# Kernel optimization log

Hardware: AMD Instinct MI355X
Metric: run time of the kernel (lower is better)

Reference implementation:

```python
import jax, jax.numpy as jnp
import numpy as np

N = 50000      # atoms
E = 800000     # edges (avg degree 32)
H = 64         # hidden_channels
F = 64         # num_filters
G = 50         # num_gaussians
L = 6          # num_interactions
B = 128        # graphs in batch
MAX_Z = 100
CUTOFF = 10.0


def setup_inputs() -> dict:
    key = jax.random.key(0)
    ks = jax.random.split(key, 20)
    s = 0.05  # weight scale
    return {
        "z": jax.random.randint(ks[0], (N,), 0, MAX_Z, dtype=jnp.int32),
        "pos": jax.random.uniform(ks[1], (N, 3), dtype=jnp.float32) * 5.0,
        "batch": jnp.sort(jax.random.randint(ks[2], (N,), 0, B, dtype=jnp.int32)),
        "edge_index": jax.random.randint(ks[3], (2, E), 0, N, dtype=jnp.int32),
        "embed": jax.random.normal(ks[4], (MAX_Z, H), dtype=jnp.float32) * s,
        "mlp_w1": jax.random.normal(ks[5], (L, G, F), dtype=jnp.float32) * s,
        "mlp_b1": jax.random.normal(ks[6], (L, F), dtype=jnp.float32) * s,
        "mlp_w2": jax.random.normal(ks[7], (L, F, F), dtype=jnp.float32) * s,
        "mlp_b2": jax.random.normal(ks[8], (L, F), dtype=jnp.float32) * s,
        "lin_w": jax.random.normal(ks[9], (L, H, F), dtype=jnp.float32) * s,
        "lin_out_w": jax.random.normal(ks[10], (L, F, H), dtype=jnp.float32) * s,
        "lin_out_b": jax.random.normal(ks[11], (L, H), dtype=jnp.float32) * s,
        "fc1_w": jax.random.normal(ks[12], (H, H // 2), dtype=jnp.float32) * s,
        "fc1_b": jax.random.normal(ks[13], (H // 2,), dtype=jnp.float32) * s,
        "fc2_w": jax.random.normal(ks[14], (H // 2, 1), dtype=jnp.float32) * s,
        "fc2_b": jax.random.normal(ks[15], (1,), dtype=jnp.float32) * s,
    }


def reference(z, pos, batch, edge_index, embed, mlp_w1, mlp_b1, mlp_w2, mlp_b2,
              lin_w, lin_out_w, lin_out_b, fc1_w, fc1_b, fc2_w, fc2_b):
    src, dst = edge_index[0], edge_index[1]
    # edge distances (replaces the python cdist loop; edge list is precomputed)
    d = jnp.sqrt(jnp.sum((pos[src] - pos[dst]) ** 2, axis=-1))  # [E]
    # Gaussian smearing
    offset = jnp.linspace(0.0, CUTOFF, G)
    coeff = -0.5 / (offset[1] - offset[0]) ** 2
    edge_attr = jnp.exp(coeff * (d[:, None] - offset) ** 2)  # [E, G]
    # cosine cutoff
    cut = 0.5 * (jnp.cos(d * np.pi / CUTOFF) + 1.0) * (d < CUTOFF).astype(d.dtype)  # [E]

    h = embed[z]  # [N, H]
    for l in range(L):
        # filter MLP on edge features, modulated by cutoff
        W = jnp.tanh(edge_attr @ mlp_w1[l] + mlp_b1[l]) @ mlp_w2[l] + mlp_b2[l]  # [E, F]
        W = W * cut[:, None]
        h_j = h @ lin_w[l]  # [N, F]
        messages = h_j[src] * W  # gather + modulate  [E, F]
        agg = jax.ops.segment_sum(messages, dst, num_segments=N)  # scatter-add [N, F]
        h = h + (agg @ lin_out_w[l] + lin_out_b[l])  # residual

    # global mean pool over graphs
    sums = jax.ops.segment_sum(h, batch, num_segments=B)  # [B, H]
    cnt = jax.ops.segment_sum(jnp.ones((h.shape[0],), h.dtype), batch, num_segments=B)
    pooled = sums / jnp.maximum(cnt, 1.0)[:, None]

    x = jax.nn.relu(pooled @ fc1_w + fc1_b)  # dropout = identity (eval)
    return x @ fc2_w + fc2_b  # [B, 1]
```

## Files before the change

kernel.cpp:

```cpp
#include <hip/hip_runtime.h>
#include <math.h>

#define E_EDGES 800000
#define N_ATOMS 50000
#define N_GRAPH 128
#define P_TBL   4096
#define SCAN_NB 49

static constexpr float PI_F   = 3.14159265358979323846f;
static constexpr float GSTEP  = 10.0f / 49.0f;
static constexpr float GCOEFF = -0.5f / (GSTEP * GSTEP);
static constexpr float DMAX   = 8.6603f;
static constexpr float DSCALE = (float)(P_TBL - 1) / DMAX;

__global__ void hist_kernel(const int* __restrict__ dst, int* __restrict__ cnt) {
    int e = blockIdx.x * 256 + threadIdx.x;
    if (e < E_EDGES) atomicAdd(&cnt[dst[e]], 1);
}

__global__ __launch_bounds__(1024)
void scan1_kernel(const int* __restrict__ cnt, int* __restrict__ local_ex,
                  int* __restrict__ bsum) {
    __shared__ int sh[1024];
    const int t = threadIdx.x;
    const int i = blockIdx.x * 1024 + t;
    const int v = (i < N_ATOMS) ? cnt[i] : 0;
    sh[t] = v;
    __syncthreads();
    #pragma unroll
    for (int off = 1; off < 1024; off <<= 1) {
        int u = (t >= off) ? sh[t - off] : 0;
        __syncthreads();
        sh[t] += u;
        __syncthreads();
    }
    if (i < N_ATOMS) local_ex[i] = sh[t] - v;
    if (t == 1023) bsum[blockIdx.x] = sh[t];
}

__global__ __launch_bounds__(1024)
void scan2_kernel(const int* __restrict__ local_ex, const int* __restrict__ bsum,
                  int* __restrict__ starts, int* __restrict__ cursor) {
    __shared__ int off;
    const int b = blockIdx.x;
    if (threadIdx.x < 64) {
        int v = (threadIdx.x < b) ? bsum[threadIdx.x] : 0;
        #pragma unroll
        for (int d = 32; d > 0; d >>= 1) v += __shfl_down(v, d, 64);
        if (threadIdx.x == 0) off = v;
    }
    __syncthreads();
    const int i = b * 1024 + threadIdx.x;
    if (i < N_ATOMS) {
        int v = local_ex[i] + off;
        starts[i] = v;
        cursor[i] = v;
    }
}

__global__ void scatter_kernel(const int* __restrict__ ei, const float* __restrict__ pos,
                               int* __restrict__ cursor, uint2* __restrict__ pk) {
    int e = blockIdx.x * 256 + threadIdx.x;
    if (e >= E_EDGES) return;
    int sidx = ei[e];
    int dd   = ei[E_EDGES + e];
    float dx = pos[3*sidx+0] - pos[3*dd+0];
    float dy = pos[3*sidx+1] - pos[3*dd+1];
    float dz = pos[3*sidx+2] - pos[3*dd+2];
    float dist = sqrtf(dx*dx + dy*dy + dz*dz);
    int p = atomicAdd(&cursor[dd], 1);
    pk[p] = make_uint2((unsigned)sidx, __float_as_uint(dist));
}

__global__ __launch_bounds__(256)
void table_kernel(const float* __restrict__ w1, const float* __restrict__ b1,
                  const float* __restrict__ w2, const float* __restrict__ b2,
                  float* __restrict__ tbl) {
    __shared__ float sa[4][52];
    __shared__ float st[4][64];
    const int l  = blockIdx.x >> 10;
    const int rb = blockIdx.x & 1023;
    const int rr = threadIdx.x >> 6;
    const int f  = threadIdx.x & 63;
    const int r  = rb * 4 + rr;
    const float dp = (float)r * (DMAX / (float)(P_TBL - 1));

    if (f < 50) {
        float t = dp - (float)f * GSTEP;
        sa[rr][f] = expf(GCOEFF * t * t);
    }
    __syncthreads();

    const float* W1 = w1 + (size_t)l * 50 * 64;
    const float* W2 = w2 + (size_t)l * 64 * 64;
    float t = b1[l * 64 + f];
    #pragma unroll 5
    for (int g = 0; g < 50; ++g) t = fmaf(sa[rr][g], W1[g * 64 + f], t);
    st[rr][f] = tanhf(t);
    __syncthreads();

    float w = b2[l * 64 + f];
    #pragma unroll 8
    for (int k = 0; k < 64; ++k) w = fmaf(st[rr][k], W2[k * 64 + f], w);
    float cutv = 0.5f * (cosf(dp * (PI_F / 10.0f)) + 1.0f);
    tbl[((size_t)l * P_TBL + r) * 64 + f] = w * cutv;
}

__global__ __launch_bounds__(256)
void embed_lin0_kernel(const int* __restrict__ z, const float* __restrict__ embed,
                       const float* __restrict__ W,
                       float* __restrict__ h, float* __restrict__ hj) {
    __shared__ float sA[64 * 65];
    __shared__ float sW[64 * 64];
    const int tid = threadIdx.x;
    const int rbase = blockIdx.x * 64;

    for (int i = tid; i < 64 * 64; i += 256) sW[i] = W[i];
    for (int i = tid; i < 64 * 64; i += 256) {
        int r = i >> 6, k = i & 63;
        int row = rbase + r;
        float v = 0.0f;
        if (row < N_ATOMS) {
            v = embed[(size_t)z[row] * 64 + k];
            h[(size_t)row * 64 + k] = v;
        }
        sA[r * 65 + k] = v;
    }
    __syncthreads();

    const int f0 = (tid & 7) * 8;
    const int r0 = (tid >> 3) * 2;
    float acc[2][8];
    #pragma unroll
    for (int i = 0; i < 2; ++i)
        #pragma unroll
        for (int j = 0; j < 8; ++j) acc[i][j] = 0.0f;

    #pragma unroll 4
    for (int k = 0; k < 64; ++k) {
        float a[2] = { sA[(r0+0)*65 + k], sA[(r0+1)*65 + k] };
        float4 wa = *(const float4*)&sW[k * 64 + f0];
        float4 wb = *(const float4*)&sW[k * 64 + f0 + 4];
        float w[8] = {wa.x, wa.y, wa.z, wa.w, wb.x, wb.y, wb.z, wb.w};
        #pragma unroll
        for (int i = 0; i < 2; ++i)
            #pragma unroll
            for (int j = 0; j < 8; ++j)
                acc[i][j] = fmaf(a[i], w[j], acc[i][j]);
    }

    #pragma unroll
    for (int i = 0; i < 2; ++i) {
        int row = rbase + r0 + i;
        if (row < N_ATOMS) {
            float* o = hj + (size_t)row * 64;
            *(float4*)&o[f0]     = make_float4(acc[i][0], acc[i][1], acc[i][2], acc[i][3]);
            *(float4*)&o[f0 + 4] = make_float4(acc[i][4], acc[i][5], acc[i][6], acc[i][7]);
        }
    }
}

__device__ __forceinline__ float edge_w(const float* __restrict__ tbl, float dist, int f) {
    float x = dist * DSCALE;
    int i0 = (int)x; i0 = (i0 > P_TBL - 2) ? (P_TBL - 2) : i0;
    float fr = x - (float)i0;
    float t0 = tbl[i0 * 64 + f];
    float t1 = tbl[i0 * 64 + 64 + f];
    return fmaf(fr, t1 - t0, t0);
}

__global__ __launch_bounds__(256)
void agg_kernel(const uint2* __restrict__ pk,
                const int* __restrict__ starts, const int* __restrict__ cnts,
                const float* __restrict__ hj, const float* __restrict__ tbl,
                float* __restrict__ agg) {
    const int f = threadIdx.x & 63;
    const int n = blockIdx.x * 4 + (threadIdx.x >> 6);
    if (n >= N_ATOMS) return;
    const int s   = starts[n];
    const int end = s + cnts[n];
    float a0 = 0.0f, a1 = 0.0f, a2 = 0.0f, a3 = 0.0f;
    float a4 = 0.0f, a5 = 0.0f, a6 = 0.0f, a7 = 0.0f;
    int e = s;
    for (; e + 8 <= end; e += 8) {
        uint2 p0 = pk[e+0], p1 = pk[e+1], p2 = pk[e+2], p3 = pk[e+3];
        uint2 p4 = pk[e+4], p5 = pk[e+5], p6 = pk[e+6], p7 = pk[e+7];
        float w0 = edge_w(tbl, __uint_as_float(p0.y), f);
        float w1 = edge_w(tbl, __uint_as_float(p1.y), f);
        float w2 = edge_w(tbl, __uint_as_float(p2.y), f);
        float w3 = edge_w(tbl, __uint_as_float(p3.y), f);
        float w4 = edge_w(tbl, __uint_as_float(p4.y), f);
        float w5 = edge_w(tbl, __uint_as_float(p5.y), f);
        float w6 = edge_w(tbl, __uint_as_float(p6.y), f);
        float w7 = edge_w(tbl, __uint_as_float(p7.y), f);
        a0 = fmaf(w0, hj[(size_t)p0.x * 64 + f], a0);
        a1 = fmaf(w1, hj[(size_t)p1.x * 64 + f], a1);
        a2 = fmaf(w2, hj[(size_t)p2.x * 64 + f], a2);
        a3 = fmaf(w3, hj[(size_t)p3.x * 64 + f], a3);
        a4 = fmaf(w4, hj[(size_t)p4.x * 64 + f], a4);
        a5 = fmaf(w5, hj[(size_t)p5.x * 64 + f], a5);
        a6 = fmaf(w6, hj[(size_t)p6.x * 64 + f], a6);
        a7 = fmaf(w7, hj[(size_t)p7.x * 64 + f], a7);
    }
    for (; e + 2 <= end; e += 2) {
        uint2 p0 = pk[e], p1 = pk[e+1];
        float w0 = edge_w(tbl, __uint_as_float(p0.y), f);
        float w1 = edge_w(tbl, __uint_as_float(p1.y), f);
        a0 = fmaf(w0, hj[(size_t)p0.x * 64 + f], a0);
        a1 = fmaf(w1, hj[(size_t)p1.x * 64 + f], a1);
    }
    if (e < end) {
        uint2 p0 = pk[e];
        float w0 = edge_w(tbl, __uint_as_float(p0.y), f);
        a0 = fmaf(w0, hj[(size_t)p0.x * 64 + f], a0);
    }
    agg[(size_t)n * 64 + f] = ((a0 + a1) + (a2 + a3)) + ((a4 + a5) + (a6 + a7));
}

__global__ __launch_bounds__(256)
void update_kernel(const float* __restrict__ agg,
                   const float* __restrict__ Wout, const float* __restrict__ bout,
                   float* __restrict__ h,
                   const float* __restrict__ Wlin, float* __restrict__ hj,
                   int doLin) {
    __shared__ float sA[64 * 65];
    __shared__ float sW[64 * 64];
    __shared__ float sb[64];
    const int tid = threadIdx.x;
    const int rbase = blockIdx.x * 64;

    for (int i = tid; i < 64 * 64; i += 256) sW[i] = Wout[i];
    if (tid < 64) sb[tid] = bout[tid];
    for (int i = tid; i < 64 * 64; i += 256) {
        int r = i >> 6, k = i & 63;
        int row = rbase + r;
        sA[r * 65 + k] = (row < N_ATOMS) ? agg[(size_t)row * 64 + k] : 0.0f;
    }
    __syncthreads();

    const int f0 = (tid & 7) * 8;
    const int r0 = (tid >> 3) * 2;

    float acc[2][8];
    #pragma unroll
    for (int i = 0; i < 2; ++i) {
        int row = rbase + r0 + i;
        if (row < N_ATOMS) {
            const float* hr = h + (size_t)row * 64;
            float4 h0 = *(const float4*)&hr[f0];
            float4 h1 = *(const float4*)&hr[f0 + 4];
            acc[i][0] = h0.x + sb[f0+0]; acc[i][1] = h0.y + sb[f0+1];
            acc[i][2] = h0.z + sb[f0+2]; acc[i][3] = h0.w + sb[f0+3];
            acc[i][4] = h1.x + sb[f0+4]; acc[i][5] = h1.y + sb[f0+5];
            acc[i][6] = h1.z + sb[f0+6]; acc[i][7] = h1.w + sb[f0+7];
        } else {
            #pragma unroll
            for (int j = 0; j < 8; ++j) acc[i][j] = 0.0f;
        }
    }

    #pragma unroll 4
    for (int k = 0; k < 64; ++k) {
        float a[2] = { sA[(r0+0)*65 + k], sA[(r0+1)*65 + k] };
        float4 wa = *(const float4*)&sW[k * 64 + f0];
        float4 wb = *(const float4*)&sW[k * 64 + f0 + 4];
        float w[8] = {wa.x, wa.y, wa.z, wa.w, wb.x, wb.y, wb.z, wb.w};
        #pragma unroll
        for (int i = 0; i < 2; ++i)
            #pragma unroll
            for (int j = 0; j < 8; ++j)
                acc[i][j] = fmaf(a[i], w[j], acc[i][j]);
    }
    __syncthreads();

    #pragma unroll
    for (int i = 0; i < 2; ++i) {
        int row = rbase + r0 + i;
        if (row < N_ATOMS) {
            float* o = h + (size_t)row * 64;
            *(float4*)&o[f0]     = make_float4(acc[i][0], acc[i][1], acc[i][2], acc[i][3]);
            *(float4*)&o[f0 + 4] = make_float4(acc[i][4], acc[i][5], acc[i][6], acc[i][7]);
        }
        #pragma unroll
        for (int j = 0; j < 8; ++j)
            sA[(r0 + i) * 65 + f0 + j] = acc[i][j];
    }
    if (!doLin) return;
    for (int i = tid; i < 64 * 64; i += 256) sW[i] = Wlin[i];
    __syncthreads();

    float acc2[2][8];
    #pragma unroll
    for (int i = 0; i < 2; ++i)
        #pragma unroll
        for (int j = 0; j < 8; ++j) acc2[i][j] = 0.0f;

    #pragma unroll 4
    for (int k = 0; k < 64; ++k) {
        float a[2] = { sA[(r0+0)*65 + k], sA[(r0+1)*65 + k] };
        float4 wa = *(const float4*)&sW[k * 64 + f0];
        float4 wb = *(const float4*)&sW[k * 64 + f0 + 4];
        float w[8] = {wa.x, wa.y, wa.z, wa.w, wb.x, wb.y, wb.z, wb.w};
        #pragma unroll
        for (int i = 0; i < 2; ++i)
            #pragma unroll
            for (int j = 0; j < 8; ++j)
                acc2[i][j] = fmaf(a[i], w[j], acc2[i][j]);
    }

    #pragma unroll
    for (int i = 0; i < 2; ++i) {
        int row = rbase + r0 + i;
        if (row < N_ATOMS) {
            float* o = hj + (size_t)row * 64;
            *(float4*)&o[f0]     = make_float4(acc2[i][0], acc2[i][1], acc2[i][2], acc2[i][3]);
            *(float4*)&o[f0 + 4] = make_float4(acc2[i][4], acc2[i][5], acc2[i][6], acc2[i][7]);
        }
    }
}

__global__ __launch_bounds__(256)
void pool_head_kernel(const float* __restrict__ h, const int* __restrict__ batch,
                      const float* __restrict__ fc1w, const float* __restrict__ fc1b,
                      const float* __restrict__ fc2w, const float* __restrict__ fc2b,
                      float* __restrict__ out) {
    __shared__ float part[4][64];
    __shared__ float sp[64];
    __shared__ float sx[32];
    __shared__ int bounds[2];
    const int g   = blockIdx.x;
    const int tid = threadIdx.x;

    if (tid < 2) {
        int target = g + tid;
        int lo = 0, hi = N_ATOMS;
        while (lo < hi) {
            int m = (lo + hi) >> 1;
            if (batch[m] < target) lo = m + 1; else hi = m;
        }
        bounds[tid] = lo;
    }
    __syncthreads();
    const int s = bounds[0], epos = bounds[1];

    const int f = tid & 63, wv = tid >> 6;
    float a = 0.0f;
    for (int r = s + wv; r < epos; r += 4) a += h[(size_t)r * 64 + f];
    part[wv][f] = a;
    __syncthreads();

    if (tid < 64) {
        float cnt = (float)(epos - s);
        sp[tid] = (part[0][tid] + part[1][tid] + part[2][tid] + part[3][tid])
                  / fmaxf(cnt, 1.0f);
    }
    __syncthreads();
    if (tid < 32) {
        float a1 = fc1b[tid];
        #pragma unroll 8
        for (int k = 0; k < 64; ++k) a1 = fmaf(sp[k], fc1w[k * 32 + tid], a1);
        sx[tid] = fmaxf(a1, 0.0f);
    }
    __syncthreads();
    if (tid == 0) {
        float a2 = fc2b[0];
        #pragma unroll 8
        for (int j = 0; j < 32; ++j) a2 = fmaf(sx[j], fc2w[j], a2);
        out[g] = a2;
    }
}

extern "C" void kernel_launch(void* const* d_in, const int* in_sizes, int n_in,
                              void* d_out, int out_size, void* d_ws, size_t ws_size,
                              hipStream_t stream) {
    const int*   z         = (const int*)  d_in[0];
    const float* pos       = (const float*)d_in[1];
    const int*   batch     = (const int*)  d_in[2];
    const int*   ei        = (const int*)  d_in[3];
    const float* embed     = (const float*)d_in[4];
    const float* mlp_w1    = (const float*)d_in[5];
    const float* mlp_b1    = (const float*)d_in[6];
    const float* mlp_w2    = (const float*)d_in[7];
    const float* mlp_b2    = (const float*)d_in[8];
    const float* lin_w     = (const float*)d_in[9];
    const float* lin_out_w = (const float*)d_in[10];
    const float* lin_out_b = (const float*)d_in[11];
    const float* fc1w      = (const float*)d_in[12];
    const float* fc1b      = (const float*)d_in[13];
    const float* fc2w      = (const float*)d_in[14];
    const float* fc2b      = (const float*)d_in[15];
    float* out = (float*)d_out;

    float* ws    = (float*)d_ws;
    float* h     = ws;
    float* hj    = h     + (size_t)N_ATOMS * 64;
    float* agg   = hj    + (size_t)N_ATOMS * 64;
    float* tbl   = agg   + (size_t)N_ATOMS * 64;
    uint2* pk    = (uint2*)(tbl + (size_t)6 * P_TBL * 64);
    int*   hist  = (int*)(pk + E_EDGES);
    int*   starts= hist  + N_ATOMS;
    int*   cursor= starts+ N_ATOMS;
    int*   lex   = cursor+ N_ATOMS;
    int*   bsum  = lex   + N_ATOMS;

    const int* dst = ei + E_EDGES;

    hipMemsetAsync(hist, 0, N_ATOMS * sizeof(int), stream);
    hist_kernel<<<E_EDGES / 256, 256, 0, stream>>>(dst, hist);
    scan1_kernel<<<SCAN_NB, 1024, 0, stream>>>(hist, lex, bsum);
    scan2_kernel<<<SCAN_NB, 1024, 0, stream>>>(lex, bsum, starts, cursor);
    scatter_kernel<<<E_EDGES / 256, 256, 0, stream>>>(ei, pos, cursor, pk);
    table_kernel<<<6 * (P_TBL / 4), 256, 0, stream>>>(mlp_w1, mlp_b1, mlp_w2, mlp_b2, tbl);

    const int ngemm_grid = (N_ATOMS + 63) / 64;
    const int agg_grid   = (N_ATOMS + 3) / 4;

    embed_lin0_kernel<<<ngemm_grid, 256, 0, stream>>>(z, embed, lin_w, h, hj);

    for (int l = 0; l < 6; ++l) {
        agg_kernel<<<agg_grid, 256, 0, stream>>>(
            pk, starts, hist, hj, tbl + (size_t)l * P_TBL * 64, agg);
        update_kernel<<<ngemm_grid, 256, 0, stream>>>(
            agg, lin_out_w + (size_t)l * 64 * 64, lin_out_b + (size_t)l * 64, h,
            (l < 5) ? (lin_w + (size_t)(l + 1) * 64 * 64) : nullptr, hj, (l < 5) ? 1 : 0);
    }

    pool_head_kernel<<<N_GRAPH, 256, 0, stream>>>(h, batch, fc1w, fc1b, fc2w, fc2b, out);
}
```

Measured before the change: 623.6 us.

## Fuse edge aggregation into per-layer update kernel with ping-pong hj buffers

Merges the gather/aggregate kernel into the update GEMM kernel, so each block aggregates its 64 atoms directly into shared memory before the output and next-layer projections. This removes the agg buffer round trip through global memory and one launch per layer. hj is double-buffered to avoid read/write races across blocks. The cost is fewer blocks (782 vs 12500) with each wave handling 16 atoms sequentially, which reduces parallelism and latency hiding for the gather-bound aggregation.

```diff
diff --git a/kernel.cpp b/kernel.cpp
--- a/kernel.cpp
+++ b/kernel.cpp
@@ -170,71 +170,69 @@
 }
 
 __global__ __launch_bounds__(256)
-void agg_kernel(const uint2* __restrict__ pk,
-                const int* __restrict__ starts, const int* __restrict__ cnts,
-                const float* __restrict__ hj, const float* __restrict__ tbl,
-                float* __restrict__ agg) {
-    const int f = threadIdx.x & 63;
-    const int n = blockIdx.x * 4 + (threadIdx.x >> 6);
-    if (n >= N_ATOMS) return;
-    const int s   = starts[n];
-    const int end = s + cnts[n];
-    float a0 = 0.0f, a1 = 0.0f, a2 = 0.0f, a3 = 0.0f;
-    float a4 = 0.0f, a5 = 0.0f, a6 = 0.0f, a7 = 0.0f;
-    int e = s;
-    for (; e + 8 <= end; e += 8) {
-        uint2 p0 = pk[e+0], p1 = pk[e+1], p2 = pk[e+2], p3 = pk[e+3];
-        uint2 p4 = pk[e+4], p5 = pk[e+5], p6 = pk[e+6], p7 = pk[e+7];
-        float w0 = edge_w(tbl, __uint_as_float(p0.y), f);
-        float w1 = edge_w(tbl, __uint_as_float(p1.y), f);
-        float w2 = edge_w(tbl, __uint_as_float(p2.y), f);
-        float w3 = edge_w(tbl, __uint_as_float(p3.y), f);
-        float w4 = edge_w(tbl, __uint_as_float(p4.y), f);
-        float w5 = edge_w(tbl, __uint_as_float(p5.y), f);
-        float w6 = edge_w(tbl, __uint_as_float(p6.y), f);
-        float w7 = edge_w(tbl, __uint_as_float(p7.y), f);
-        a0 = fmaf(w0, hj[(size_t)p0.x * 64 + f], a0);
-        a1 = fmaf(w1, hj[(size_t)p1.x * 64 + f], a1);
-        a2 = fmaf(w2, hj[(size_t)p2.x * 64 + f], a2);
-        a3 = fmaf(w3, hj[(size_t)p3.x * 64 + f], a3);
-        a4 = fmaf(w4, hj[(size_t)p4.x * 64 + f], a4);
-        a5 = fmaf(w5, hj[(size_t)p5.x * 64 + f], a5);
-        a6 = fmaf(w6, hj[(size_t)p6.x * 64 + f], a6);
-        a7 = fmaf(w7, hj[(size_t)p7.x * 64 + f], a7);
-    }
-    for (; e + 2 <= end; e += 2) {
-        uint2 p0 = pk[e], p1 = pk[e+1];
-        float w0 = edge_w(tbl, __uint_as_float(p0.y), f);
-        float w1 = edge_w(tbl, __uint_as_float(p1.y), f);
-        a0 = fmaf(w0, hj[(size_t)p0.x * 64 + f], a0);
-        a1 = fmaf(w1, hj[(size_t)p1.x * 64 + f], a1);
-    }
-    if (e < end) {
-        uint2 p0 = pk[e];
-        float w0 = edge_w(tbl, __uint_as_float(p0.y), f);
-        a0 = fmaf(w0, hj[(size_t)p0.x * 64 + f], a0);
-    }
-    agg[(size_t)n * 64 + f] = ((a0 + a1) + (a2 + a3)) + ((a4 + a5) + (a6 + a7));
-}
-
-__global__ __launch_bounds__(256)
-void update_kernel(const float* __restrict__ agg,
-                   const float* __restrict__ Wout, const float* __restrict__ bout,
-                   float* __restrict__ h,
-                   const float* __restrict__ Wlin, float* __restrict__ hj,
-                   int doLin) {
+void layer_kernel(const uint2* __restrict__ pk,
+                  const int* __restrict__ starts, const int* __restrict__ cnts,
+                  const float* __restrict__ hj_in, const float* __restrict__ tbl,
+                  const float* __restrict__ Wout, const float* __restrict__ bout,
+                  float* __restrict__ h,
+                  const float* __restrict__ Wlin, float* __restrict__ hj_out,
+                  int doLin) {
     __shared__ float sA[64 * 65];
     __shared__ float sW[64 * 64];
     __shared__ float sb[64];
     const int tid = threadIdx.x;
     const int rbase = blockIdx.x * 64;
+    const int f  = tid & 63;
+    const int wv = tid >> 6;
 
     for (int i = tid; i < 64 * 64; i += 256) sW[i] = Wout[i];
     if (tid < 64) sb[tid] = bout[tid];
-    for (int i = tid; i < 64 * 64; i += 256) {
-        int r = i >> 6, k = i & 63;
-        int row = rbase + r;
-        sA[r * 65 + k] = (row < N_ATOMS) ? agg[(size_t)row * 64 + k] : 0.0f;
+
+    for (int i = 0; i < 16; ++i) {
+        const int r = wv * 16 + i;
+        const int n = rbase + r;
+        float res = 0.0f;
+        if (n < N_ATOMS) {
+            const int s   = starts[n];
+            const int end = s + cnts[n];
+            float a0 = 0.0f, a1 = 0.0f, a2 = 0.0f, a3 = 0.0f;
+            float a4 = 0.0f, a5 = 0.0f, a6 = 0.0f, a7 = 0.0f;
+            int e = s;
+            for (; e + 8 <= end; e += 8) {
+                uint2 p0 = pk[e+0], p1 = pk[e+1], p2 = pk[e+2], p3 = pk[e+3];
+                uint2 p4 = pk[e+4], p5 = pk[e+5], p6 = pk[e+6], p7 = pk[e+7];
+                float w0 = edge_w(tbl, __uint_as_float(p0.y), f);
+                float w1 = edge_w(tbl, __uint_as_float(p1.y), f);
+                float w2 = edge_w(tbl, __uint_as_float(p2.y), f);
+                float w3 = edge_w(tbl, __uint_as_float(p3.y), f);
+                float w4 = edge_w(tbl, __uint_as_float(p4.y), f);
+                float w5 = edge_w(tbl, __uint_as_float(p5.y), f);
+                float w6 = edge_w(tbl, __uint_as_float(p6.y), f);
+                float w7 = edge_w(tbl, __uint_as_float(p7.y), f);
+                a0 = fmaf(w0, hj_in[(size_t)p0.x * 64 + f], a0);
+                a1 = fmaf(w1, hj_in[(size_t)p1.x * 64 + f], a1);
+                a2 = fmaf(w2, hj_in[(size_t)p2.x * 64 + f], a2);
+                a3 = fmaf(w3, hj_in[(size_t)p3.x * 64 + f], a3);
+                a4 = fmaf(w4, hj_in[(size_t)p4.x * 64 + f], a4);
+                a5 = fmaf(w5, hj_in[(size_t)p5.x * 64 + f], a5);
+                a6 = fmaf(w6, hj_in[(size_t)p6.x * 64 + f], a6);
+                a7 = fmaf(w7, hj_in[(size_t)p7.x * 64 + f], a7);
+            }
+            for (; e + 2 <= end; e += 2) {
+                uint2 p0 = pk[e], p1 = pk[e+1];
+                float w0 = edge_w(tbl, __uint_as_float(p0.y), f);
+                float w1 = edge_w(tbl, __uint_as_float(p1.y), f);
+                a0 = fmaf(w0, hj_in[(size_t)p0.x * 64 + f], a0);
+                a1 = fmaf(w1, hj_in[(size_t)p1.x * 64 + f], a1);
+            }
+            if (e < end) {
+                uint2 p0 = pk[e];
+                float w0 = edge_w(tbl, __uint_as_float(p0.y), f);
+                a0 = fmaf(w0, hj_in[(size_t)p0.x * 64 + f], a0);
+            }
+            res = ((a0 + a1) + (a2 + a3)) + ((a4 + a5) + (a6 + a7));
+        }
+        sA[r * 65 + f] = res;
     }
     __syncthreads();
 
@@ -312,7 +310,7 @@
     for (int i = 0; i < 2; ++i) {
         int row = rbase + r0 + i;
         if (row < N_ATOMS) {
-            float* o = hj + (size_t)row * 64;
+            float* o = hj_out + (size_t)row * 64;
             *(float4*)&o[f0]     = make_float4(acc2[i][0], acc2[i][1], acc2[i][2], acc2[i][3]);
             *(float4*)&o[f0 + 4] = make_float4(acc2[i][4], acc2[i][5], acc2[i][6], acc2[i][7]);
         }
@@ -393,9 +391,9 @@
 
     float* ws    = (float*)d_ws;
     float* h     = ws;
-    float* hj    = h     + (size_t)N_ATOMS * 64;
-    float* agg   = hj    + (size_t)N_ATOMS * 64;
-    float* tbl   = agg   + (size_t)N_ATOMS * 64;
+    float* hj0   = h     + (size_t)N_ATOMS * 64;
+    float* hj1   = hj0   + (size_t)N_ATOMS * 64;
+    float* tbl   = hj1   + (size_t)N_ATOMS * 64;
     uint2* pk    = (uint2*)(tbl + (size_t)6 * P_TBL * 64);
     int*   hist  = (int*)(pk + E_EDGES);
     int*   starts= hist  + N_ATOMS;
@@ -413,16 +411,16 @@
     table_kernel<<<6 * (P_TBL / 4), 256, 0, stream>>>(mlp_w1, mlp_b1, mlp_w2, mlp_b2, tbl);
 
     const int ngemm_grid = (N_ATOMS + 63) / 64;
-    const int agg_grid   = (N_ATOMS + 3) / 4;
-
-    embed_lin0_kernel<<<ngemm_grid, 256, 0, stream>>>(z, embed, lin_w, h, hj);
-
+
+    embed_lin0_kernel<<<ngemm_grid, 256, 0, stream>>>(z, embed, lin_w, h, hj0);
+
+    float* hjbuf[2] = { hj0, hj1 };
     for (int l = 0; l < 6; ++l) {
-        agg_kernel<<<agg_grid, 256, 0, stream>>>(
-            pk, starts, hist, hj, tbl + (size_t)l * P_TBL * 64, agg);
-        update_kernel<<<ngemm_grid, 256, 0, stream>>>(
-            agg, lin_out_w + (size_t)l * 64 * 64, lin_out_b + (size_t)l * 64, h,
-            (l < 5) ? (lin_w + (size_t)(l + 1) * 64 * 64) : nullptr, hj, (l < 5) ? 1 : 0);
+        layer_kernel<<<ngemm_grid, 256, 0, stream>>>(
+            pk, starts, hist, hjbuf[l & 1], tbl + (size_t)l * P_TBL * 64,
+            lin_out_w + (size_t)l * 64 * 64, lin_out_b + (size_t)l * 64, h,
+            (l < 5) ? (lin_w + (size_t)(l + 1) * 64 * 64) : nullptr,
+            hjbuf[(l + 1) & 1], (l < 5) ? 1 : 0);
     }
 
     pool_head_kernel<<<N_GRAPH, 256, 0, stream>>>(h, batch, fc1w, fc1b, fc2w, fc2b, out);
```

Measured after the change: 717.4 us. 1.15x slower.
